# Performance work log

Measured on AMD Instinct MI355X. Metric: run time of the kernel, lower is better.

The kernel has to match this reference:

```python
import jax, jax.numpy as jnp
import numpy as np
from jax import lax

FEAT_STRIDE = 16
ANCHOR_SCALES = (8, 16, 32)
RATIOS = (0.5, 1.0, 2.0)
A = 9                      # 3 scales * 3 ratios
PRE_NMS = 6000
POST_NMS = 300
NMS_THRESH = 0.7
MIN_SIZE = 16
POOL = 7
SPATIAL_SCALE = 1.0 / 16.0
N_CLASSES = 32


def _generate_anchors():
    base = 16.0
    xc = yc = (base - 1.0) / 2.0
    size = base * base
    ratios = np.array(RATIOS)
    scales = np.array(ANCHOR_SCALES, dtype=np.float64)
    ws = np.round(np.sqrt(size / ratios))
    hs = np.round(ws * ratios)
    def mk(w, h, cx, cy):
        return np.stack([cx - 0.5 * (w - 1), cy - 0.5 * (h - 1),
                         cx + 0.5 * (w - 1), cy + 0.5 * (h - 1)], 1)
    ratio_anchors = mk(ws, hs, xc, yc)
    out = []
    for a in ratio_anchors:
        aw = a[2] - a[0] + 1
        ah = a[3] - a[1] + 1
        acx = a[0] + 0.5 * (aw - 1)
        acy = a[1] + 0.5 * (ah - 1)
        out.append(mk(aw * scales, ah * scales, acx, acy))
    return np.concatenate(out, 0).astype(np.float32)  # [9,4]


def _conv(x, w, b, pad):
    y = lax.conv_general_dilated(x, w, (1, 1), [(pad, pad), (pad, pad)],
                                 dimension_numbers=('NCHW', 'OIHW', 'NCHW'))
    return y + b[None, :, None, None]


def _bbox_transform_inv(boxes, deltas):
    w = boxes[:, 2] - boxes[:, 0] + 1.0
    h = boxes[:, 3] - boxes[:, 1] + 1.0
    cx = boxes[:, 0] + 0.5 * w
    cy = boxes[:, 1] + 0.5 * h
    dx, dy, dw, dh = deltas[:, 0], deltas[:, 1], deltas[:, 2], deltas[:, 3]
    pcx = dx * w + cx
    pcy = dy * h + cy
    pw = jnp.exp(dw) * w
    ph = jnp.exp(dh) * h
    return jnp.stack([pcx - 0.5 * pw, pcy - 0.5 * ph,
                      pcx + 0.5 * pw, pcy + 0.5 * ph], 1)


def _nms(boxes, scores):
    # greedy NMS, fixed POST_NMS picks; self-IoU (=1) suppresses the picked box
    areas = (boxes[:, 2] - boxes[:, 0] + 1.0) * (boxes[:, 3] - boxes[:, 1] + 1.0)
    def body(sc, _):
        i = jnp.argmax(sc)
        b = boxes[i]
        xx1 = jnp.maximum(b[0], boxes[:, 0])
        yy1 = jnp.maximum(b[1], boxes[:, 1])
        xx2 = jnp.minimum(b[2], boxes[:, 2])
        yy2 = jnp.minimum(b[3], boxes[:, 3])
        inter = jnp.maximum(xx2 - xx1 + 1.0, 0.0) * jnp.maximum(yy2 - yy1 + 1.0, 0.0)
        iou = inter / (areas[i] + areas - inter)
        return jnp.where(iou > NMS_THRESH, -jnp.inf, sc), i
    _, keep = lax.scan(body, scores, None, length=POST_NMS)
    return keep


def _proposal_layer(cls_prob, bbox_pred, img_info):
    B, _, H, W = cls_prob.shape
    anchors = jnp.asarray(_generate_anchors())                       # [9,4]
    sx = (np.arange(W) * FEAT_STRIDE).astype(np.float32)
    sy = (np.arange(H) * FEAT_STRIDE).astype(np.float32)
    sxg, syg = np.meshgrid(sx, sy)                                   # [H,W]
    shifts = jnp.asarray(np.stack([sxg.ravel(), syg.ravel(),
                                   sxg.ravel(), syg.ravel()], 1))     # [H*W,4]
    all_anchors = (shifts[:, None, :] + anchors[None, :, :]).reshape(-1, 4)  # (h,w,a)
    scores = jnp.transpose(cls_prob[0, A:], (1, 2, 0)).reshape(-1)   # fg probs, (h,w,a)
    deltas = jnp.transpose(bbox_pred[0], (1, 2, 0)).reshape(-1, 4)
    props = _bbox_transform_inv(all_anchors, deltas)
    im_h, im_w, im_scale = img_info[0], img_info[1], img_info[2]
    x1 = jnp.clip(props[:, 0], 0.0, im_w - 1.0)
    y1 = jnp.clip(props[:, 1], 0.0, im_h - 1.0)
    x2 = jnp.clip(props[:, 2], 0.0, im_w - 1.0)
    y2 = jnp.clip(props[:, 3], 0.0, im_h - 1.0)
    props = jnp.stack([x1, y1, x2, y2], 1)
    ok = ((x2 - x1 + 1.0) >= MIN_SIZE * im_scale) & ((y2 - y1 + 1.0) >= MIN_SIZE * im_scale)
    scores = jnp.where(ok, scores, -jnp.inf)
    order = jnp.argsort(-scores)[:PRE_NMS]
    pb, ps = props[order], scores[order]
    keep = _nms(pb, ps)
    return pb[keep]                                                   # [POST_NMS,4]


def _roi_pool(feat, rois):
    # legacy torch RoIPool(7,7,1/16) math: rounded roi coords, floor/ceil bins, max pool, 0 for empty bins
    C, H, W = feat.shape
    hh = jnp.arange(H, dtype=feat.dtype)
    ww = jnp.arange(W, dtype=feat.dtype)
    p = jnp.arange(POOL, dtype=feat.dtype)
    NEG = jnp.asarray(-1e30, feat.dtype)
    def one(roi):
        rsw = jnp.round(roi[0] * SPATIAL_SCALE)
        rsh = jnp.round(roi[1] * SPATIAL_SCALE)
        rew = jnp.round(roi[2] * SPATIAL_SCALE)
        reh = jnp.round(roi[3] * SPATIAL_SCALE)
        bw = jnp.maximum(rew - rsw + 1.0, 1.0) / POOL
        bh = jnp.maximum(reh - rsh + 1.0, 1.0) / POOL
        hs = jnp.clip(jnp.floor(p * bh) + rsh, 0, H)
        he = jnp.clip(jnp.ceil((p + 1) * bh) + rsh, 0, H)
        ws_ = jnp.clip(jnp.floor(p * bw) + rsw, 0, W)
        we = jnp.clip(jnp.ceil((p + 1) * bw) + rsw, 0, W)
        mh = (hh[None, :] >= hs[:, None]) & (hh[None, :] < he[:, None])  # [7,H]
        mw = (ww[None, :] >= ws_[:, None]) & (ww[None, :] < we[:, None])  # [7,W]
        t = jnp.where(mw[:, None, None, :], feat[None], NEG).max(-1)      # [7pw,C,H]
        pooled = jnp.where(mh[:, None, None, :], t[None], NEG).max(-1)    # [7ph,7pw,C]
        pooled = jnp.where(pooled < -1e29, 0.0, pooled)                   # empty bin -> 0
        return jnp.transpose(pooled, (2, 0, 1))                           # [C,7,7]
    return lax.map(one, rois)


def setup_inputs() -> dict:
    key = jax.random.key(0)
    ks = jax.random.split(key, 8)
    f32 = jnp.float32
    rn = lambda k, s, sc=0.01: jax.random.normal(k, s, dtype=f32) * sc
    return {
        'img_features': jax.random.normal(ks[0], (1, 512, 38, 63), dtype=f32),
        'img_info': jnp.array([600.0, 1000.0, 1.0], dtype=f32),
        'conv1_w': rn(ks[1], (512, 512, 3, 3)),
        'conv1_b': jnp.zeros((512,), f32),
        'score_w': rn(ks[2], (2 * A, 512, 1, 1), 0.1),
        'score_b': jnp.zeros((2 * A,), f32),
        'bbox_w': rn(ks[3], (4 * A, 512, 1, 1)),
        'bbox_b': jnp.zeros((4 * A,), f32),
        'fc6_w': rn(ks[4], (4096, 512 * POOL * POOL)),
        'fc6_b': jnp.zeros((4096,), f32),
        'fc7_w': rn(ks[5], (4096, 4096)),
        'fc7_b': jnp.zeros((4096,), f32),
        'score_fc_w': rn(ks[6], (N_CLASSES, 4096)),
        'score_fc_b': jnp.zeros((N_CLASSES,), f32),
        'bbox_fc_w': rn(ks[7], (4 * N_CLASSES, 4096)),
        'bbox_fc_b': jnp.zeros((4 * N_CLASSES,), f32),
    }


def reference(img_features, img_info, conv1_w, conv1_b, score_w, score_b,
              bbox_w, bbox_b, fc6_w, fc6_b, fc7_w, fc7_b,
              score_fc_w, score_fc_b, bbox_fc_w, bbox_fc_b):
    B, C, H, W = img_features.shape
    # RPN head
    rpn_conv = jax.nn.relu(_conv(img_features, conv1_w, conv1_b, 1))
    cls_score = _conv(rpn_conv, score_w, score_b, 0)                  # [1,18,H,W]
    # reshape_layer(x,2) -> softmax over dim 1 -> reshape back
    prob = jax.nn.softmax(cls_score.reshape(B, 2, A * H, W), axis=1).reshape(B, 2 * A, H, W)
    bbox_pred = _conv(rpn_conv, bbox_w, bbox_b, 0)                    # [1,36,H,W]
    # proposal layer is non-differentiable in the original (cpu/numpy)
    rois = lax.stop_gradient(
        _proposal_layer(lax.stop_gradient(prob), lax.stop_gradient(bbox_pred), img_info))
    # RoIPool + FC head (eval mode: dropout is identity)
    pooled = _roi_pool(img_features[0], rois).reshape(POST_NMS, -1)   # [300, 25088]
    x = jax.nn.relu(pooled @ fc6_w.T + fc6_b)
    x = jax.nn.relu(x @ fc7_w.T + fc7_b)
    cls = x @ score_fc_w.T + score_fc_b
    cls_prob = jax.nn.softmax(cls, axis=1)
    box = x @ bbox_fc_w.T + bbox_fc_b
    return cls_prob, box, rois
```

## Files before the change

### kernel.cpp

```cpp
#include <hip/hip_runtime.h>
#include <cstdint>
#include <cstddef>

#define H_FEAT 38
#define W_FEAT 63
#define NPIX   2394
#define NANCH  21546
#define NSORT  32768
#define PRE_NMS_K 6000
#define POST_NMS_K 300
#define KCONV  4608
#define NMS_TH 0.7f
#define MPAD   320
#define NW64   94
#define NPAD   6016

typedef __bf16 bf16_t;
typedef bf16_t bf16x8 __attribute__((ext_vector_type(8)));
typedef float  f32x4  __attribute__((ext_vector_type(4)));

__device__ __forceinline__ size_t packed_off(int row, int k, int RT) {
  return ((size_t)(k >> 5) * RT + (row >> 4)) * 512 +
         (size_t)(((row & 15) << 5) + (((k >> 3) & 3) << 3) + (k & 7));
}

__device__ const float ANCHORS[9][4] = {
  { -84.f, -40.f,  99.f,  55.f}, {-176.f, -88.f, 191.f, 103.f}, {-360.f,-184.f, 375.f, 199.f},
  { -56.f, -56.f,  71.f,  71.f}, {-120.f,-120.f, 135.f, 135.f}, {-248.f,-248.f, 263.f, 263.f},
  { -36.f, -80.f,  51.f,  95.f}, { -80.f,-168.f,  95.f, 183.f}, {-168.f,-344.f, 183.f, 359.f}};

#define BM 64
#define BN 64
#define BK 16

template<int AMODE>
__launch_bounds__(256)
__global__ void gemm_nt(const float* __restrict__ A, const float* __restrict__ W,
                        const float* __restrict__ bias, float* __restrict__ C,
                        int M, int N, int K, int relu) {
  __shared__ float As[BK][BM];
  __shared__ float Bs[BK][BN];
  const int tid = threadIdx.x;
  const int m0 = blockIdx.y * BM;
  const int n0 = blockIdx.x * BN;
  const int lr = tid >> 2;
  const int lk = (tid & 3) * 4;
  const int ty = tid >> 4, tx = tid & 15;
  const int gm = m0 + lr;
  const int ph = gm / W_FEAT, pw = gm - (gm / W_FEAT) * W_FEAT;

  auto loadA = [&](int k0) -> float4 {
    if (AMODE == 0) {
      return (gm < M) ? *(const float4*)(A + (size_t)gm * K + k0 + lk)
                      : make_float4(0.f, 0.f, 0.f, 0.f);
    } else {
      float t[4];
      if (gm < M) {
#pragma unroll
        for (int q = 0; q < 4; ++q) {
          int k = k0 + lk + q;
          int ic = k / 9, tap = k - ic * 9;
          int hh = ph + tap / 3 - 1, ww = pw + (tap % 3) - 1;
          t[q] = (hh >= 0 && hh < H_FEAT && ww >= 0 && ww < W_FEAT)
                   ? A[(ic * H_FEAT + hh) * W_FEAT + ww] : 0.f;
        }
      } else { t[0] = t[1] = t[2] = t[3] = 0.f; }
      return make_float4(t[0], t[1], t[2], t[3]);
    }
  };
  auto loadB = [&](int k0) -> float4 {
    return *(const float4*)(W + (size_t)(n0 + lr) * K + k0 + lk);
  };

  float acc[4][4] = {};
  float4 av = loadA(0), bv = loadB(0);
  for (int k0 = 0; k0 < K; k0 += BK) {
    __syncthreads();
    As[lk + 0][lr] = av.x; As[lk + 1][lr] = av.y; As[lk + 2][lr] = av.z; As[lk + 3][lr] = av.w;
    Bs[lk + 0][lr] = bv.x; Bs[lk + 1][lr] = bv.y; Bs[lk + 2][lr] = bv.z; Bs[lk + 3][lr] = bv.w;
    __syncthreads();
    if (k0 + BK < K) { av = loadA(k0 + BK); bv = loadB(k0 + BK); }
#pragma unroll
    for (int kk = 0; kk < BK; ++kk) {
      float4 a = *(const float4*)&As[kk][ty * 4];
      float4 b = *(const float4*)&Bs[kk][tx * 4];
      float ar[4] = {a.x, a.y, a.z, a.w}, br[4] = {b.x, b.y, b.z, b.w};
#pragma unroll
      for (int i = 0; i < 4; ++i)
#pragma unroll
        for (int j = 0; j < 4; ++j) acc[i][j] += ar[i] * br[j];
    }
  }
  float4 bb = *(const float4*)(bias + n0 + tx * 4);
  float bb4[4] = {bb.x, bb.y, bb.z, bb.w};
#pragma unroll
  for (int i = 0; i < 4; ++i) {
    int om = m0 + ty * 4 + i;
    if (om < M) {
      float o[4];
#pragma unroll
      for (int j = 0; j < 4; ++j) {
        o[j] = acc[i][j] + bb4[j];
        if (relu) o[j] = fmaxf(o[j], 0.f);
      }
      *(float4*)(C + (size_t)om * N + n0 + tx * 4) = make_float4(o[0], o[1], o[2], o[3]);
    }
  }
}

__global__ void pack_w_bf16(const float* __restrict__ W, bf16_t* __restrict__ P,
                            int K, int total) {
  int gid = blockIdx.x * blockDim.x + threadIdx.x;
  if (gid >= total) return;
  int q = gid & 3;
  int t = gid >> 2;
  int l = t & 15; t >>= 4;
  int rt = t & 255;
  int ks = t >> 8;
  int row = (rt << 4) | l;
  int k = (ks << 5) + (q << 3);
  const float* src = W + (size_t)row * K + k;
  f32x4 va = *(const f32x4*)src;
  f32x4 vb = *(const f32x4*)(src + 4);
  bf16x8 o;
#pragma unroll
  for (int j = 0; j < 4; ++j) { o[j] = (bf16_t)va[j]; o[j + 4] = (bf16_t)vb[j]; }
  *(bf16x8*)(P + (size_t)gid * 8) = o;
}

__launch_bounds__(256)
__global__ void gemm_mfma_p(const bf16_t* __restrict__ Ap, const bf16_t* __restrict__ Wp,
                            float* __restrict__ Cp, int MT, int NT, int N, int kSteps,
                            size_t sliceElems) {
  const int tid = threadIdx.x;
  const int wave = tid >> 6, lane = tid & 63;
  const int l15 = lane & 15, quad = lane >> 4;
  const int wm = wave & 1, wn = wave >> 1;
  const int m0 = blockIdx.y * 64 + wm * 32;
  const int n0 = blockIdx.x * 64 + wn * 32;
  const int z = blockIdx.z;
  const int ks0 = z * kSteps;

  const size_t lofs = (size_t)((l15 << 5) + (quad << 3));
  const bf16_t* a0 = Ap + ((size_t)ks0 * MT + (m0 >> 4)) * 512 + lofs;
  const bf16_t* w0 = Wp + ((size_t)ks0 * NT + (n0 >> 4)) * 512 + lofs;
  const size_t strideA = (size_t)MT * 512, strideW = (size_t)NT * 512;

  f32x4 acc00 = {0.f, 0.f, 0.f, 0.f}, acc01 = acc00, acc10 = acc00, acc11 = acc00;

  for (int ks = 0; ks < kSteps; ++ks) {
    bf16x8 af0 = *(const bf16x8*)a0;
    bf16x8 af1 = *(const bf16x8*)(a0 + 512);
    bf16x8 bf0 = *(const bf16x8*)w0;
    bf16x8 bf1 = *(const bf16x8*)(w0 + 512);
    acc00 = __builtin_amdgcn_mfma_f32_16x16x32_bf16(af0, bf0, acc00, 0, 0, 0);
    acc01 = __builtin_amdgcn_mfma_f32_16x16x32_bf16(af0, bf1, acc01, 0, 0, 0);
    acc10 = __builtin_amdgcn_mfma_f32_16x16x32_bf16(af1, bf0, acc10, 0, 0, 0);
    acc11 = __builtin_amdgcn_mfma_f32_16x16x32_bf16(af1, bf1, acc11, 0, 0, 0);
    a0 += strideA; w0 += strideW;
  }

  float* Cz = Cp + (size_t)z * sliceElems;
  const int rb = m0 + quad * 4;
#pragma unroll
  for (int i = 0; i < 4; ++i) {
    Cz[(size_t)(rb + i) * N + n0 + l15]           = acc00[i];
    Cz[(size_t)(rb + i) * N + n0 + 16 + l15]      = acc01[i];
    Cz[(size_t)(rb + 16 + i) * N + n0 + l15]      = acc10[i];
    Cz[(size_t)(rb + 16 + i) * N + n0 + 16 + l15] = acc11[i];
  }
}

__launch_bounds__(256)
__global__ void gemm_mfma(const bf16_t* __restrict__ A, const float* __restrict__ Wt,
                          float* __restrict__ Cp, int K, int N, int kSteps,
                          size_t sliceElems) {
  const int tid = threadIdx.x;
  const int wave = tid >> 6, lane = tid & 63;
  const int l15 = lane & 15, quad = lane >> 4;
  const int wm = wave & 1, wn = wave >> 1;
  const int m0 = blockIdx.y * 64 + wm * 32;
  const int n0 = blockIdx.x * 64 + wn * 32;
  const int z = blockIdx.z;
  const int kb = z * kSteps * 32;

  const bf16_t* a0 = A + (size_t)(m0 + l15) * K + kb + quad * 8;
  const bf16_t* a1 = a0 + (size_t)16 * K;
  const float*  w0 = Wt + (size_t)(n0 + l15) * K + kb + quad * 8;
  const float*  w1 = w0 + (size_t)16 * K;

  f32x4 acc00 = {0.f, 0.f, 0.f, 0.f}, acc01 = acc00, acc10 = acc00, acc11 = acc00;

  for (int ks = 0; ks < kSteps; ++ks) {
    bf16x8 af0 = *(const bf16x8*)a0;
    bf16x8 af1 = *(const bf16x8*)a1;
    f32x4 b0a = *(const f32x4*)w0;
    f32x4 b0b = *(const f32x4*)(w0 + 4);
    f32x4 b1a = *(const f32x4*)w1;
    f32x4 b1b = *(const f32x4*)(w1 + 4);
    bf16x8 bf0, bf1;
#pragma unroll
    for (int j = 0; j < 4; ++j) {
      bf0[j] = (bf16_t)b0a[j]; bf0[j + 4] = (bf16_t)b0b[j];
      bf1[j] = (bf16_t)b1a[j]; bf1[j + 4] = (bf16_t)b1b[j];
    }
    acc00 = __builtin_amdgcn_mfma_f32_16x16x32_bf16(af0, bf0, acc00, 0, 0, 0);
    acc01 = __builtin_amdgcn_mfma_f32_16x16x32_bf16(af0, bf1, acc01, 0, 0, 0);
    acc10 = __builtin_amdgcn_mfma_f32_16x16x32_bf16(af1, bf0, acc10, 0, 0, 0);
    acc11 = __builtin_amdgcn_mfma_f32_16x16x32_bf16(af1, bf1, acc11, 0, 0, 0);
    a0 += 32; a1 += 32; w0 += 32; w1 += 32;
  }

  float* Cz = Cp + (size_t)z * sliceElems;
  const int rb = m0 + quad * 4;
#pragma unroll
  for (int i = 0; i < 4; ++i) {
    Cz[(size_t)(rb + i) * N + n0 + l15]           = acc00[i];
    Cz[(size_t)(rb + i) * N + n0 + 16 + l15]      = acc01[i];
    Cz[(size_t)(rb + 16 + i) * N + n0 + l15]      = acc10[i];
    Cz[(size_t)(rb + 16 + i) * N + n0 + 16 + l15] = acc11[i];
  }
}

__global__ void epilogue_k(const float* __restrict__ Cp, size_t sliceElems, int KS,
                           const float* __restrict__ bias, int M, int N,
                           float* __restrict__ out_f32, bf16_t* __restrict__ out_bf16,
                           int relu, int packB) {
  int idx = blockIdx.x * blockDim.x + threadIdx.x;
  if (idx >= M * N) return;
  int m = idx / N, n = idx - m * N;
  float s = 0.f;
  for (int z = 0; z < KS; ++z) s += Cp[(size_t)z * sliceElems + idx];
  s += bias[n];
  if (relu) s = fmaxf(s, 0.f);
  if (out_f32)  out_f32[idx] = s;
  if (out_bf16) {
    size_t o = packB ? packed_off(m, n, MPAD / 16) : (size_t)idx;
    out_bf16[o] = (bf16_t)s;
  }
}

__global__ void gemv_nt(const float* __restrict__ A, const float* __restrict__ W,
                        const float* __restrict__ bias, float* __restrict__ C,
                        int M, int N, int K, int relu) {
  int gid = blockIdx.x * blockDim.x + threadIdx.x;
  if (gid >= M * N) return;
  int m = gid / N, n = gid - m * N;
  const float* a = A + (size_t)m * K;
  const float* w = W + (size_t)n * K;
  float acc = 0.f;
  for (int k = 0; k < K; k += 4) {
    float4 x = *(const float4*)(a + k);
    float4 y = *(const float4*)(w + k);
    acc += x.x * y.x + x.y * y.y + x.z * y.z + x.w * y.w;
  }
  float o = acc + bias[n];
  if (relu) o = fmaxf(o, 0.f);
  C[gid] = o;
}

__device__ inline unsigned flip_f32(float f) {
  unsigned u = __float_as_uint(f);
  return (u & 0x80000000u) ? ~u : (u | 0x80000000u);
}

__global__ void proposal_prep(const float* __restrict__ cls,
                              const float* __restrict__ bbox,
                              const float* __restrict__ info,
                              float* __restrict__ props,
                              float* __restrict__ scores,
                              unsigned long long* __restrict__ keys) {
  int idx = blockIdx.x * blockDim.x + threadIdx.x;
  if (idx >= NSORT) return;
  unsigned long long key = 0ull;
  if (idx < NANCH) {
    int a = idx % 9, m = idx / 9;
    int h = m / W_FEAT, w = m - (m / W_FEAT) * W_FEAT;
    float s0 = cls[m * 18 + a], s1 = cls[m * 18 + 9 + a];
    float mx = fmaxf(s0, s1);
    float e0 = expf(s0 - mx), e1 = expf(s1 - mx);
    float sc = e1 / (e0 + e1);
    const float* d = bbox + m * 36 + a * 4;
    float dx = d[0], dy = d[1], dw = d[2], dh = d[3];
    float ax1 = ANCHORS[a][0] + w * 16.f, ay1 = ANCHORS[a][1] + h * 16.f;
    float ax2 = ANCHORS[a][2] + w * 16.f, ay2 = ANCHORS[a][3] + h * 16.f;
    float aw = ax2 - ax1 + 1.f, ah = ay2 - ay1 + 1.f;
    float cx = ax1 + 0.5f * aw, cy = ay1 + 0.5f * ah;
    float pcx = dx * aw + cx, pcy = dy * ah + cy;
    float pww = expf(dw) * aw, phh = expf(dh) * ah;
    float x1 = pcx - 0.5f * pww, y1 = pcy - 0.5f * phh;
    float x2 = pcx + 0.5f * pww, y2 = pcy + 0.5f * phh;
    float imh = info[0], imw = info[1], iscale = info[2];
    x1 = fminf(fmaxf(x1, 0.f), imw - 1.f);
    y1 = fminf(fmaxf(y1, 0.f), imh - 1.f);
    x2 = fminf(fmaxf(x2, 0.f), imw - 1.f);
    y2 = fminf(fmaxf(y2, 0.f), imh - 1.f);
    bool ok = (x2 - x1 + 1.f >= 16.f * iscale) && (y2 - y1 + 1.f >= 16.f * iscale);
    float s = ok ? sc : -INFINITY;
    *(float4*)(props + 4 * idx) = make_float4(x1, y1, x2, y2);
    scores[idx] = s;
    key = ((unsigned long long)flip_f32(s) << 32) |
          (unsigned long long)(0xFFFFFFFFu - (unsigned)idx);
  }
  keys[idx] = key;
}

__global__ void bitonic_global(unsigned long long* __restrict__ keys, int j, int k) {
  int i = blockIdx.x * blockDim.x + threadIdx.x;
  int l = i ^ j;
  if (l > i) {
    unsigned long long a = keys[i], b = keys[l];
    bool up = ((i & k) == 0);
    if (up ? (a < b) : (a > b)) { keys[i] = b; keys[l] = a; }
  }
}

__launch_bounds__(1024)
__global__ void bitonic_lds(unsigned long long* __restrict__ keys, int jstart, int k) {
  __shared__ unsigned long long s[2048];
  const int tid = threadIdx.x;
  const int base = blockIdx.x * 2048;
  s[tid] = keys[base + tid];
  s[tid + 1024] = keys[base + tid + 1024];
  __syncthreads();
  for (int j = jstart; j > 0; j >>= 1) {
    int il = ((tid & ~(j - 1)) << 1) | (tid & (j - 1));
    int ig = base + il;
    bool up = ((ig & k) == 0);
    unsigned long long a = s[il], b = s[il + j];
    if (up ? (a < b) : (a > b)) { s[il] = b; s[il + j] = a; }
    __syncthreads();
  }
  keys[base + tid] = s[tid];
  keys[base + tid + 1024] = s[tid + 1024];
}

__global__ void nms_gather(const unsigned long long* __restrict__ keys,
                           const float* __restrict__ props,
                           const float* __restrict__ scores,
                           float4* __restrict__ sbox, float* __restrict__ sarea,
                           float* __restrict__ sscore,
                           unsigned long long* __restrict__ vmask) {
  int j = blockIdx.x * blockDim.x + threadIdx.x;
  bool valid = false;
  float4 b = make_float4(0.f, 0.f, 0.f, 0.f);
  float s = -INFINITY, area = 0.f;
  if (j < PRE_NMS_K) {
    unsigned long long k = keys[j];
    unsigned orig = 0xFFFFFFFFu - (unsigned)(k & 0xFFFFFFFFull);
    b = *(const float4*)(props + 4 * (size_t)orig);
    s = scores[orig];
    area = (b.z - b.x + 1.f) * (b.w - b.y + 1.f);
    valid = (s != -INFINITY);
  }
  if (j < NPAD) { sbox[j] = b; sarea[j] = area; sscore[j] = s; }
  unsigned long long ball = __ballot(valid);
  if ((threadIdx.x & 63) == 0 && j < NPAD) vmask[j >> 6] = ball;
}

__global__ void nms_mask(const float4* __restrict__ sbox, const float* __restrict__ sarea,
                         unsigned long long* __restrict__ mask) {
  int idx = blockIdx.x * blockDim.x + threadIdx.x;
  if (idx >= NPAD * NW64) return;
  int j = idx / NW64, w = idx - j * NW64;
  float4 bj = sbox[j];
  float aj = sarea[j];
  unsigned long long m = 0ull;
  int kbase = w * 64;
#pragma unroll 8
  for (int b = 0; b < 64; ++b) {
    int k = kbase + b;
    float4 bk = sbox[k];
    float xx1 = fmaxf(bj.x, bk.x), yy1 = fmaxf(bj.y, bk.y);
    float xx2 = fminf(bj.z, bk.z), yy2 = fminf(bj.w, bk.w);
    float iw = fmaxf(xx2 - xx1 + 1.f, 0.f), ih = fmaxf(yy2 - yy1 + 1.f, 0.f);
    float inter = iw * ih;
    float iou = inter / (aj + sarea[k] - inter);
    if (iou > NMS_TH) m |= (1ull << b);
  }
  mask[(size_t)j * NW64 + w] = m;
}

__launch_bounds__(64)
__global__ void nms_scan(const float4* __restrict__ sbox,
                         const unsigned long long* __restrict__ vmask,
                         const unsigned long long* __restrict__ mask,
                         float* __restrict__ rois_out) {
  const int lane = threadIdx.x;
  const int w0 = 2 * lane, w1 = 2 * lane + 1;
  unsigned long long S0 = 0ull, S1 = 0ull;
  const unsigned long long V0 = (w0 < NW64) ? vmask[w0] : 0ull;
  const unsigned long long V1 = (w1 < NW64) ? vmask[w1] : 0ull;
  __shared__ int keepIdx[POST_NMS_K];
  int keeps = 0;
  for (int w = 0; w < NW64 && keeps < POST_NMS_K; ++w) {
    const int owner = w >> 1;
    unsigned long long candsrc = (w & 1) ? ((~S1) & V1) : ((~S0) & V0);
    unsigned long long cw = __shfl(candsrc, owner);
    while (cw) {
      int b = __builtin_ctzll(cw);
      int j = w * 64 + b;
      if (lane == 0) keepIdx[keeps] = j;
      keeps++;
      if (keeps == POST_NMS_K) break;
      const unsigned long long* row = mask + (size_t)j * NW64;
      if (w0 < NW64) S0 |= row[w0];
      if (w1 < NW64) S1 |= row[w1];
      candsrc = (w & 1) ? ((~S1) & V1) : ((~S0) & V0);
      unsigned long long hi = (b == 63) ? 0ull : (~0ull << (b + 1));
      cw = __shfl(candsrc, owner) & hi;
    }
  }
  __syncthreads();
  for (int t = lane; t < POST_NMS_K; t += 64) {
    int j = (t < keeps) ? keepIdx[t] : 0;
    float4 bx = sbox[j];
    *(float4*)(rois_out + 4 * t) = bx;
  }
}

template<int PACK>
__global__ void roi_pool(const float* __restrict__ feat,
                         const float* __restrict__ rois,
                         bf16_t* __restrict__ out) {
  const int r = blockIdx.x;
  const float4 roi = *(const float4*)(rois + 4 * r);
  float rsw = rintf(roi.x * 0.0625f);
  float rsh = rintf(roi.y * 0.0625f);
  float rew = rintf(roi.z * 0.0625f);
  float reh = rintf(roi.w * 0.0625f);
  float bw = fmaxf(rew - rsw + 1.f, 1.f) / 7.f;
  float bh = fmaxf(reh - rsh + 1.f, 1.f) / 7.f;
  for (int idx = threadIdx.x; idx < 512 * 49; idx += blockDim.x) {
    int c = idx / 49, b = idx - c * 49;
    int ph = b / 7, pw = b - ph * 7;
    float hs = fminf(fmaxf(floorf(ph * bh) + rsh, 0.f), (float)H_FEAT);
    float he = fminf(fmaxf(ceilf((ph + 1) * bh) + rsh, 0.f), (float)H_FEAT);
    float wS = fminf(fmaxf(floorf(pw * bw) + rsw, 0.f), (float)W_FEAT);
    float wE = fminf(fmaxf(ceilf((pw + 1) * bw) + rsw, 0.f), (float)W_FEAT);
    int h0 = (int)hs, h1 = (int)he, w0 = (int)wS, w1 = (int)wE;
    float m = -1e30f;
    const float* fc = feat + (size_t)c * (H_FEAT * W_FEAT);
    for (int h = h0; h < h1; ++h)
      for (int w = w0; w < w1; ++w)
        m = fmaxf(m, fc[h * W_FEAT + w]);
    size_t o = PACK ? packed_off(r, idx, MPAD / 16) : ((size_t)r * 25088 + idx);
    out[o] = (bf16_t)((m < -1e29f) ? 0.f : m);
  }
}

__global__ void softmax32(const float* __restrict__ in, float* __restrict__ out) {
  int r = blockIdx.x * blockDim.x + threadIdx.x;
  if (r >= POST_NMS_K) return;
  const float* x = in + r * 32;
  float m = x[0];
#pragma unroll
  for (int k = 1; k < 32; ++k) m = fmaxf(m, x[k]);
  float e[32]; float s = 0.f;
#pragma unroll
  for (int k = 0; k < 32; ++k) { e[k] = expf(x[k] - m); s += e[k]; }
  float inv = 1.f / s;
#pragma unroll
  for (int k = 0; k < 32; ++k) out[r * 32 + k] = e[k] * inv;
}

extern "C" void kernel_launch(void* const* d_in, const int* in_sizes, int n_in,
                              void* d_out, int out_size, void* d_ws, size_t ws_size,
                              hipStream_t stream) {
  const float* feat    = (const float*)d_in[0];
  const float* info    = (const float*)d_in[1];
  const float* conv1_w = (const float*)d_in[2];
  const float* conv1_b = (const float*)d_in[3];
  const float* score_w = (const float*)d_in[4];
  const float* score_b = (const float*)d_in[5];
  const float* bbox_w  = (const float*)d_in[6];
  const float* bbox_b  = (const float*)d_in[7];
  const float* fc6_w   = (const float*)d_in[8];
  const float* fc6_b   = (const float*)d_in[9];
  const float* fc7_w   = (const float*)d_in[10];
  const float* fc7_b   = (const float*)d_in[11];
  const float* sfc_w   = (const float*)d_in[12];
  const float* sfc_b   = (const float*)d_in[13];
  const float* bfc_w   = (const float*)d_in[14];
  const float* bfc_b   = (const float*)d_in[15];
  float* out = (float*)d_out;
  char*  ws  = (char*)d_ws;

  size_t off = 0;
  auto alloc = [&](size_t bytes) { size_t o = off; off += (bytes + 255) & ~(size_t)255; return o; };
  float* cls    = (float*)(ws + alloc((size_t)NPIX * 18 * 4));
  float* bbx    = (float*)(ws + alloc((size_t)NPIX * 36 * 4));
  float* props  = (float*)(ws + alloc((size_t)NANCH * 4 * 4));
  float* scores = (float*)(ws + alloc((size_t)NANCH * 4));
  unsigned long long* keys = (unsigned long long*)(ws + alloc((size_t)NSORT * 8));
  float* rpn    = (float*)(ws + alloc((size_t)NPIX * 512 * 4));
  char*  pooled_raw = ws + alloc((size_t)MPAD * 25088 * 2);
  bf16_t* pooled = (bf16_t*)pooled_raw;
  float*  fc7P   = (float*)pooled_raw;
  float*  fc7o   = fc7P;
  float* fc6P    = (float*)(ws + alloc((size_t)4 * MPAD * 4096 * 4));
  bf16_t* fc6bf  = (bf16_t*)(ws + alloc((size_t)MPAD * 4096 * 2));
  float* clsfc   = (float*)(ws + alloc((size_t)POST_NMS_K * 32 * 4));

  char* nmsbase = (char*)fc6P;
  float4* sbox  = (float4*)nmsbase;
  float*  sarea = (float*)(nmsbase + 96256);
  float*  sscore= (float*)(nmsbase + 120320);
  unsigned long long* vmask = (unsigned long long*)(nmsbase + 144384);
  unsigned long long* maskb = (unsigned long long*)(nmsbase + 145408);

  bf16_t* fc6wp = (bf16_t*)(ws + alloc((size_t)4096 * 25088 * 2));
  bf16_t* fc7wp = (bf16_t*)(ws + alloc((size_t)4096 * 4096 * 2));
  const bool packed = (off <= ws_size);

  float* rois_out = out + 9600 + 38400;

  gemm_nt<1><<<dim3(512 / BN, (NPIX + BM - 1) / BM), 256, 0, stream>>>(
      feat, conv1_w, conv1_b, rpn, NPIX, 512, KCONV, 1);
  gemv_nt<<<(NPIX * 18 + 255) / 256, 256, 0, stream>>>(rpn, score_w, score_b, cls, NPIX, 18, 512, 0);
  gemv_nt<<<(NPIX * 36 + 255) / 256, 256, 0, stream>>>(rpn, bbox_w, bbox_b, bbx, NPIX, 36, 512, 0);
  proposal_prep<<<NSORT / 256, 256, 0, stream>>>(cls, bbx, info, props, scores, keys);
  for (int k = 2; k <= 2048; k <<= 1)
    bitonic_lds<<<NSORT / 2048, 1024, 0, stream>>>(keys, k >> 1, k);
  for (int k = 4096; k <= NSORT; k <<= 1) {
    for (int j = k >> 1; j >= 2048; j >>= 1)
      bitonic_global<<<NSORT / 256, 256, 0, stream>>>(keys, j, k);
    bitonic_lds<<<NSORT / 2048, 1024, 0, stream>>>(keys, 1024, k);
  }
  nms_gather<<<(NPAD + 255) / 256, 256, 0, stream>>>(keys, props, scores, sbox, sarea, sscore, vmask);
  nms_mask<<<(NPAD * NW64 + 255) / 256, 256, 0, stream>>>(sbox, sarea, maskb);
  nms_scan<<<1, 64, 0, stream>>>(sbox, vmask, maskb, rois_out);

  if (packed) {
    pack_w_bf16<<<(4096 * 25088 / 8) / 256, 256, 0, stream>>>(fc6_w, fc6wp, 25088, 4096 * 25088 / 8);
    pack_w_bf16<<<(4096 * 4096 / 8) / 256, 256, 0, stream>>>(fc7_w, fc7wp, 4096, 4096 * 4096 / 8);
    roi_pool<1><<<POST_NMS_K, 256, 0, stream>>>(feat, rois_out, pooled);
    gemm_mfma_p<<<dim3(64, MPAD / 64, 4), 256, 0, stream>>>(
        pooled, fc6wp, fc6P, MPAD / 16, 256, 4096, 25088 / 32 / 4, (size_t)MPAD * 4096);
    epilogue_k<<<(POST_NMS_K * 4096 + 255) / 256, 256, 0, stream>>>(
        fc6P, (size_t)MPAD * 4096, 4, fc6_b, POST_NMS_K, 4096, nullptr, fc6bf, 1, 1);
    gemm_mfma_p<<<dim3(64, MPAD / 64, 2), 256, 0, stream>>>(
        fc6bf, fc7wp, fc7P, MPAD / 16, 256, 4096, 4096 / 32 / 2, (size_t)MPAD * 4096);
    epilogue_k<<<(POST_NMS_K * 4096 + 255) / 256, 256, 0, stream>>>(
        fc7P, (size_t)MPAD * 4096, 2, fc7_b, POST_NMS_K, 4096, fc7o, nullptr, 1, 0);
  } else {
    roi_pool<0><<<POST_NMS_K, 256, 0, stream>>>(feat, rois_out, pooled);
    gemm_mfma<<<dim3(64, MPAD / 64, 4), 256, 0, stream>>>(
        pooled, fc6_w, fc6P, 25088, 4096, 25088 / 32 / 4, (size_t)MPAD * 4096);
    epilogue_k<<<(POST_NMS_K * 4096 + 255) / 256, 256, 0, stream>>>(
        fc6P, (size_t)MPAD * 4096, 4, fc6_b, POST_NMS_K, 4096, nullptr, fc6bf, 1, 0);
    gemm_mfma<<<dim3(64, MPAD / 64, 2), 256, 0, stream>>>(
        fc6bf, fc7_w, fc7P, 4096, 4096, 4096 / 32 / 2, (size_t)MPAD * 4096);
    epilogue_k<<<(POST_NMS_K * 4096 + 255) / 256, 256, 0, stream>>>(
        fc7P, (size_t)MPAD * 4096, 2, fc7_b, POST_NMS_K, 4096, fc7o, nullptr, 1, 0);
  }
  gemv_nt<<<(POST_NMS_K * 32 + 255) / 256, 256, 0, stream>>>(fc7o, sfc_w, sfc_b, clsfc, POST_NMS_K, 32, 4096, 0);
  softmax32<<<(POST_NMS_K + 63) / 64, 64, 0, stream>>>(clsfc, out);
  gemv_nt<<<(POST_NMS_K * 128 + 255) / 256, 256, 0, stream>>>(fc7o, bfc_w, bfc_b, out + 9600, POST_NMS_K, 128, 4096, 0);
}
```

Before: 2.537 ms.

## Transpose features to HWC and parallelize RoI pooling per bin

Adds a tiled transpose kernel that converts the feature map from CHW to HWC layout, then replaces the per-ROI pooling kernel with one that launches a block per (bin, ROI). Each thread reads four contiguous channels with vector loads, so memory accesses are coalesced and the grid gets far more parallelism than 300 blocks. The cost is an extra transpose pass and workspace buffer, plus scattered bf16 stores into the packed layout.

```diff
diff --git a/kernel.cpp b/kernel.cpp
--- a/kernel.cpp
+++ b/kernel.cpp
@@ -419,7 +419,63 @@
   }
 }
 
-template<int PACK>
+__launch_bounds__(256)
+__global__ void transpose_feat(const float* __restrict__ in, float* __restrict__ out) {
+  __shared__ float tile[32][33];
+  const int p0 = blockIdx.x * 32;
+  const int c0 = blockIdx.y * 32;
+  const int tx = threadIdx.x & 31, ty = threadIdx.x >> 5;
+#pragma unroll
+  for (int i = 0; i < 32; i += 8) {
+    int c = c0 + ty + i, p = p0 + tx;
+    tile[ty + i][tx] = (p < NPIX) ? in[(size_t)c * NPIX + p] : 0.f;
+  }
+  __syncthreads();
+#pragma unroll
+  for (int i = 0; i < 32; i += 8) {
+    int p = p0 + ty + i, c = c0 + tx;
+    if (p < NPIX) out[(size_t)p * 512 + c] = tile[tx][ty + i];
+  }
+}
+
+__launch_bounds__(128)
+__global__ void roi_pool_p(const float* __restrict__ feat_t,
+                           const float* __restrict__ rois,
+                           bf16_t* __restrict__ out) {
+  const int b = blockIdx.x;
+  const int r = blockIdx.y;
+  const int ph = b / 7, pw = b - ph * 7;
+  const float4 roi = *(const float4*)(rois + 4 * r);
+  float rsw = rintf(roi.x * 0.0625f);
+  float rsh = rintf(roi.y * 0.0625f);
+  float rew = rintf(roi.z * 0.0625f);
+  float reh = rintf(roi.w * 0.0625f);
+  float bw = fmaxf(rew - rsw + 1.f, 1.f) / 7.f;
+  float bh = fmaxf(reh - rsh + 1.f, 1.f) / 7.f;
+  float hs = fminf(fmaxf(floorf(ph * bh) + rsh, 0.f), (float)H_FEAT);
+  float he = fminf(fmaxf(ceilf((ph + 1) * bh) + rsh, 0.f), (float)H_FEAT);
+  float wS = fminf(fmaxf(floorf(pw * bw) + rsw, 0.f), (float)W_FEAT);
+  float wE = fminf(fmaxf(ceilf((pw + 1) * bw) + rsw, 0.f), (float)W_FEAT);
+  const int h0 = (int)hs, h1 = (int)he, w0 = (int)wS, w1 = (int)wE;
+  const int c = threadIdx.x * 4;
+  f32x4 m = {-1e30f, -1e30f, -1e30f, -1e30f};
+  for (int h = h0; h < h1; ++h) {
+    const float* rowp = feat_t + ((size_t)(h * W_FEAT) + w0) * 512 + c;
+    for (int w = w0; w < w1; ++w) {
+      f32x4 v = *(const f32x4*)rowp;
+#pragma unroll
+      for (int j = 0; j < 4; ++j) m[j] = fmaxf(m[j], v[j]);
+      rowp += 512;
+    }
+  }
+  const int RT = MPAD / 16;
+#pragma unroll
+  for (int j = 0; j < 4; ++j) {
+    float v = (m[j] < -1e29f) ? 0.f : m[j];
+    out[packed_off(r, (c + j) * 49 + b, RT)] = (bf16_t)v;
+  }
+}
+
 __global__ void roi_pool(const float* __restrict__ feat,
                          const float* __restrict__ rois,
                          bf16_t* __restrict__ out) {
@@ -444,8 +500,7 @@
     for (int h = h0; h < h1; ++h)
       for (int w = w0; w < w1; ++w)
         m = fmaxf(m, fc[h * W_FEAT + w]);
-    size_t o = PACK ? packed_off(r, idx, MPAD / 16) : ((size_t)r * 25088 + idx);
-    out[o] = (bf16_t)((m < -1e29f) ? 0.f : m);
+    out[(size_t)r * 25088 + idx] = (bf16_t)((m < -1e29f) ? 0.f : m);
   }
 }
 
@@ -501,6 +556,7 @@
   float* fc6P    = (float*)(ws + alloc((size_t)4 * MPAD * 4096 * 4));
   bf16_t* fc6bf  = (bf16_t*)(ws + alloc((size_t)MPAD * 4096 * 2));
   float* clsfc   = (float*)(ws + alloc((size_t)POST_NMS_K * 32 * 4));
+  float* feat_t  = (float*)(ws + alloc((size_t)NPIX * 512 * 4));
 
   char* nmsbase = (char*)fc6P;
   float4* sbox  = (float4*)nmsbase;
@@ -534,7 +590,8 @@
   if (packed) {
     pack_w_bf16<<<(4096 * 25088 / 8) / 256, 256, 0, stream>>>(fc6_w, fc6wp, 25088, 4096 * 25088 / 8);
     pack_w_bf16<<<(4096 * 4096 / 8) / 256, 256, 0, stream>>>(fc7_w, fc7wp, 4096, 4096 * 4096 / 8);
-    roi_pool<1><<<POST_NMS_K, 256, 0, stream>>>(feat, rois_out, pooled);
+    transpose_feat<<<dim3((NPIX + 31) / 32, 16), 256, 0, stream>>>(feat, feat_t);
+    roi_pool_p<<<dim3(49, POST_NMS_K), 128, 0, stream>>>(feat_t, rois_out, pooled);
     gemm_mfma_p<<<dim3(64, MPAD / 64, 4), 256, 0, stream>>>(
         pooled, fc6wp, fc6P, MPAD / 16, 256, 4096, 25088 / 32 / 4, (size_t)MPAD * 4096);
     epilogue_k<<<(POST_NMS_K * 4096 + 255) / 256, 256, 0, stream>>>(
@@ -544,7 +601,7 @@
     epilogue_k<<<(POST_NMS_K * 4096 + 255) / 256, 256, 0, stream>>>(
         fc7P, (size_t)MPAD * 4096, 2, fc7_b, POST_NMS_K, 4096, fc7o, nullptr, 1, 0);
   } else {
-    roi_pool<0><<<POST_NMS_K, 256, 0, stream>>>(feat, rois_out, pooled);
+    roi_pool<<<POST_NMS_K, 256, 0, stream>>>(feat, rois_out, pooled);
     gemm_mfma<<<dim3(64, MPAD / 64, 4), 256, 0, stream>>>(
         pooled, fc6_w, fc6P, 25088, 4096, 25088 / 32 / 4, (size_t)MPAD * 4096);
     epilogue_k<<<(POST_NMS_K * 4096 + 255) / 256, 256, 0, stream>>>(
```

Result: faster. 2.166 ms (-14.6%).
